# Kernel optimization log

Hardware: AMD Instinct MI355X
Metric: run time of the kernel (lower is better)

Reference implementation:

```python
import jax, jax.numpy as jnp
import numpy as np

N_NODES = 100000
N_EDGES = 800000
IN_F = 128
HID = 128
OUT_F = 64


def setup_inputs() -> dict:
    key = jax.random.key(0)
    ks = jax.random.split(key, 13)
    s = 1.0 / np.sqrt(HID)
    return {
        "x": jax.random.normal(ks[0], (N_NODES, IN_F), jnp.float32),
        "src": jax.random.randint(ks[1], (N_EDGES,), 0, N_NODES, jnp.int32),
        "dst": jax.random.randint(ks[2], (N_EDGES,), 0, N_NODES, jnp.int32),
        "W1": jax.random.normal(ks[3], (HID, IN_F), jnp.float32) * s,
        "b1": jax.random.normal(ks[4], (HID,), jnp.float32) * s,
        "W2": jax.random.normal(ks[5], (HID, HID), jnp.float32) * s,
        "b2": jax.random.normal(ks[6], (HID,), jnp.float32) * s,
        "W3": jax.random.normal(ks[7], (HID, HID), jnp.float32) * s,
        "b3": jax.random.normal(ks[8], (HID,), jnp.float32) * s,
        "Wo1": jax.random.normal(ks[9], (HID, HID), jnp.float32) * s,
        "bo1": jax.random.normal(ks[10], (HID,), jnp.float32) * s,
        "Wo2": jax.random.normal(ks[11], (OUT_F, HID), jnp.float32) * s,
        "bo2": jax.random.normal(ks[12], (OUT_F,), jnp.float32) * s,
    }


def _mean_agg(h, src, dst, n_nodes):
    # mean over incoming edges (DGL copy_u -> mean reducer); isolated nodes get 0
    summed = jax.ops.segment_sum(h[src], dst, num_segments=n_nodes)
    deg = jax.ops.segment_sum(jnp.ones_like(src, h.dtype), dst, num_segments=n_nodes)
    return summed / jnp.maximum(deg, 1.0)[:, None]


def _lin(h, W, b):
    return h @ W.T + b


def reference(x, src, dst, W1, b1, W2, b2, W3, b3, Wo1, bo1, Wo2, bo2):
    n = x.shape[0]
    # x1 = fc1(x); x = relu(x1); x2 = fc2(x)
    x2 = _lin(jax.nn.relu(_lin(x, W1, b1)), W2, b2)
    # gin1: apply_func = Sequential(fc1, relu, fc2) on (x2 + mean_agg(x2)), eps=0
    h = x2 + _mean_agg(x2, src, dst, n)
    h = _lin(jax.nn.relu(_lin(h, W1, b1)), W2, b2)
    # x3 = fc3(h); h = relu(x3)
    h = jax.nn.relu(_lin(h, W3, b3))
    # gin2: apply_func = Sequential(fc3, relu) on (h + mean_agg(h))
    h = h + _mean_agg(h, src, dst, n)
    h = jax.nn.relu(_lin(h, W3, b3))
    # output head
    h = jax.nn.relu(_lin(h, Wo1, bo1))
    return _lin(h, Wo2, bo2)
```

## Files before the change

kernel.cpp:

```cpp
#include <hip/hip_runtime.h>

#define NNODES 100000
#define NEDGES 800000
#define NTILE128 782
#define NROWPAD (NTILE128*128)

typedef _Float16 f16x8 __attribute__((ext_vector_type(8)));
typedef float    f32x4 __attribute__((ext_vector_type(4)));
typedef unsigned int u32;
typedef unsigned short u16;

__global__ __launch_bounds__(256) void hist_kernel(const int* __restrict__ dst,
                                                   int* __restrict__ counts, int nE) {
    int i = blockIdx.x * 256 + threadIdx.x;
    if (i < nE) atomicAdd(counts + dst[i], 1);
}

__global__ __launch_bounds__(256) void scan1_kernel(const int* __restrict__ counts,
                                                    int* __restrict__ bsum, int n) {
    __shared__ int s[256];
    int i = blockIdx.x * 256 + threadIdx.x;
    s[threadIdx.x] = (i < n) ? counts[i] : 0;
    __syncthreads();
    for (int off = 128; off > 0; off >>= 1) {
        if (threadIdx.x < off) s[threadIdx.x] += s[threadIdx.x + off];
        __syncthreads();
    }
    if (threadIdx.x == 0) bsum[blockIdx.x] = s[0];
}

__global__ __launch_bounds__(512) void scan2_kernel(int* __restrict__ bsum, int nb) {
    __shared__ int s[512];
    int t = threadIdx.x;
    int orig = (t < nb) ? bsum[t] : 0;
    s[t] = orig;
    __syncthreads();
    for (int off = 1; off < 512; off <<= 1) {
        int v = (t >= off) ? s[t - off] : 0;
        __syncthreads();
        s[t] += v;
        __syncthreads();
    }
    if (t < nb) bsum[t] = s[t] - orig;
}

__global__ __launch_bounds__(256) void scan3_kernel(int* __restrict__ counts,
                                                    const int* __restrict__ boff,
                                                    int* __restrict__ rowptr, int n) {
    __shared__ int s[256];
    int i = blockIdx.x * 256 + threadIdx.x;
    int t = threadIdx.x;
    int orig = (i < n) ? counts[i] : 0;
    s[t] = orig;
    __syncthreads();
    for (int off = 1; off < 256; off <<= 1) {
        int v = (t >= off) ? s[t - off] : 0;
        __syncthreads();
        s[t] += v;
        __syncthreads();
    }
    if (i < n) {
        rowptr[i] = boff[blockIdx.x] + s[t] - orig;
        counts[i] = 0;
    }
    if (i == n - 1) rowptr[n] = boff[blockIdx.x] + s[t];
}

__global__ __launch_bounds__(256) void fill_kernel(const int* __restrict__ src,
                                                   const int* __restrict__ dst,
                                                   const int* __restrict__ rowptr,
                                                   int* __restrict__ cur,
                                                   int* __restrict__ eidx, int nE) {
    int i = blockIdx.x * 256 + threadIdx.x;
    if (i >= nE) return;
    int d = dst[i];
    int p = atomicAdd(cur + d, 1);
    eidx[rowptr[d] + p] = src[i];
}

__global__ __launch_bounds__(256) void wpack_kernel(const float* __restrict__ W1,
                                                    const float* __restrict__ W2,
                                                    const float* __restrict__ W3,
                                                    const float* __restrict__ Wo1,
                                                    const float* __restrict__ Wo2,
                                                    _Float16* __restrict__ wp) {
    int i = blockIdx.x * 256 + threadIdx.x;
    if (i >= 9216) return;
    const float* Wm;
    int li;
    size_t base;
    if (i < 8192) {
        int m = i >> 11;
        li = i & 2047;
        Wm = (m == 0) ? W1 : (m == 1) ? W2 : (m == 2) ? W3 : Wo1;
        base = (size_t)m * 16384;
    } else {
        li = i - 8192;
        Wm = Wo2;
        base = 65536;
    }
    int lane = li & 63;
    int n = ((li >> 8) * 16) + (lane & 15);
    int k0 = (((li >> 6) & 3) * 32) + ((lane >> 4) * 8);
    const float* s = Wm + (size_t)n * 128 + k0;
    float4 a = *(const float4*)s;
    float4 b = *(const float4*)(s + 4);
    f16x8 v;
    v[0] = (_Float16)a.x; v[1] = (_Float16)a.y; v[2] = (_Float16)a.z; v[3] = (_Float16)a.w;
    v[4] = (_Float16)b.x; v[5] = (_Float16)b.y; v[6] = (_Float16)b.z; v[7] = (_Float16)b.w;
    *(f16x8*)(wp + base + (size_t)li * 8) = v;
}

__global__ __launch_bounds__(256) void gather_kernel(const _Float16* __restrict__ H,
                                                     const int* __restrict__ rowptr,
                                                     const int* __restrict__ eidx,
                                                     _Float16* __restrict__ O, int n) {
    int node = blockIdx.x * 4 + (threadIdx.x >> 6);
    int lane = threadIdx.x & 63;
    if (node >= n) return;
    int g = lane >> 4, p = lane & 15;
    int e0 = rowptr[node], e1 = rowptr[node + 1];
    float acc[8] = {0.f, 0.f, 0.f, 0.f, 0.f, 0.f, 0.f, 0.f};
    for (int j = e0; j < e1; j += 8) {
        int na = e1 - j;
        int sid = (lane < 8 && lane < na) ? eidx[j + lane] : -1;
        int s0 = __shfl(sid, g);
        int s1 = __shfl(sid, g + 4);
        f16x8 v0, v1;
        bool h0 = (s0 >= 0), h1 = (s1 >= 0);
        if (h0) v0 = *(const f16x8*)(H + (size_t)s0 * 128 + p * 8);
        if (h1) v1 = *(const f16x8*)(H + (size_t)s1 * 128 + p * 8);
        if (h0) {
#pragma unroll
            for (int r = 0; r < 8; ++r) acc[r] += (float)v0[r];
        }
        if (h1) {
#pragma unroll
            for (int r = 0; r < 8; ++r) acc[r] += (float)v1[r];
        }
    }
#pragma unroll
    for (int r = 0; r < 8; ++r) {
        acc[r] += __shfl_xor(acc[r], 16);
        acc[r] += __shfl_xor(acc[r], 32);
    }
    if (g == 0) {
        float rinv = 1.0f / fmaxf((float)(e1 - e0), 1.0f);
        f16x8 b = *(const f16x8*)(H + (size_t)node * 128 + p * 8);
        f16x8 o;
#pragma unroll
        for (int r = 0; r < 8; ++r) o[r] = (_Float16)((float)b[r] + acc[r] * rinv);
        *(f16x8*)(O + (size_t)node * 128 + p * 8) = o;
    }
}

template <int S, bool INF32, bool OUTF32, int TL, bool R0, bool R1, bool R2>
__global__ __launch_bounds__(512, 2) void chain_kernel(
    const void* __restrict__ A_,
    const _Float16* __restrict__ wq0, const float* __restrict__ Bg0,
    const _Float16* __restrict__ wq1, const float* __restrict__ Bg1,
    const _Float16* __restrict__ wq2, const float* __restrict__ Bg2,
    _Float16* __restrict__ O, float* __restrict__ Of32) {
    __shared__ u32 ibuf[128][137];
    const int tid = threadIdx.x;
    const int lane = tid & 63, w = tid >> 6;
    const int lm = lane & 15, g = lane >> 4;
    const int tile = blockIdx.x;

    f16x8 ah[4];
    const int arow = tile * 128 + w * 16 + lm;
    if (INF32) {
        const float* base = (const float*)A_ + (size_t)min(arow, NNODES - 1) * 128;
#pragma unroll
        for (int ks = 0; ks < 4; ++ks) {
            float4 a = *(const float4*)(base + ks * 32 + g * 8);
            float4 b = *(const float4*)(base + ks * 32 + g * 8 + 4);
            ah[ks][0] = (_Float16)a.x; ah[ks][1] = (_Float16)a.y;
            ah[ks][2] = (_Float16)a.z; ah[ks][3] = (_Float16)a.w;
            ah[ks][4] = (_Float16)b.x; ah[ks][5] = (_Float16)b.y;
            ah[ks][6] = (_Float16)b.z; ah[ks][7] = (_Float16)b.w;
        }
    } else {
        const _Float16* bp = (const _Float16*)A_ + (size_t)arow * 128;
#pragma unroll
        for (int ks = 0; ks < 4; ++ks) ah[ks] = *(const f16x8*)(bp + ks * 32 + g * 8);
    }

#pragma unroll
    for (int s = 0; s < S; ++s) {
        const _Float16* wq = (s == 0) ? wq0 : (s == 1) ? wq1 : wq2;
        const float* Bg = (s == 0) ? Bg0 : (s == 1) ? Bg1 : Bg2;
        const bool RELU = (s == 0) ? R0 : (s == 1) ? R1 : R2;
        const int T = (s == S - 1) ? TL : 8;

        f32x4 acc[8];
#pragma unroll
        for (int t = 0; t < 8; ++t)
            if (t < T) {
                float bv = Bg[t * 16 + lm];
                acc[t] = (f32x4){bv, bv, bv, bv};
            }
#pragma unroll
        for (int t = 0; t < 8; ++t)
            if (t < T) {
#pragma unroll
                for (int ks = 0; ks < 4; ++ks) {
                    f16x8 wv = *(const f16x8*)(wq + ((size_t)(t * 4 + ks) * 64 + lane) * 8);
                    acc[t] = __builtin_amdgcn_mfma_f32_16x16x32_f16(ah[ks], wv, acc[t], 0, 0, 0);
                }
            }

        if (s < S - 1) {
            __syncthreads();
            const int lrow0 = w * 16 + g * 4;
#pragma unroll
            for (int t = 0; t < 8; ++t)
#pragma unroll
                for (int r = 0; r < 4; ++r) {
                    float v = acc[t][r];
                    if (RELU) v = fmaxf(v, 0.f);
                    _Float16 h = (_Float16)v;
                    ibuf[lrow0 + r][t * 16 + lm] = (u32)(*(u16*)&h);
                }
            __syncthreads();
            const u32* rp = &ibuf[w * 16 + lm][0];
#pragma unroll
            for (int ks = 0; ks < 4; ++ks) {
                u32 v[8];
                *(f32x4*)v = *(const f32x4*)(rp + ks * 32 + g * 8);
                *(f32x4*)(v + 4) = *(const f32x4*)(rp + ks * 32 + g * 8 + 4);
#pragma unroll
                for (int j = 0; j < 8; ++j) {
                    u16 hs = (u16)(v[j] & 0xffffu);
                    ah[ks][j] = *(_Float16*)&hs;
                }
            }
        } else if (OUTF32) {
            const int mrow0 = tile * 128 + w * 16 + g * 4;
#pragma unroll
            for (int t = 0; t < TL; ++t) {
                const int n = t * 16 + lm;
#pragma unroll
                for (int r = 0; r < 4; ++r) {
                    float v = acc[t][r];
                    if (RELU) v = fmaxf(v, 0.f);
                    int m = mrow0 + r;
                    if (m < NNODES) Of32[(size_t)m * 64 + n] = v;
                }
            }
        } else {
            __syncthreads();
            const int lrow0 = w * 16 + g * 4;
#pragma unroll
            for (int t = 0; t < 8; ++t)
#pragma unroll
                for (int r = 0; r < 4; ++r) {
                    float v = acc[t][r];
                    if (RELU) v = fmaxf(v, 0.f);
                    _Float16 h = (_Float16)v;
                    ibuf[lrow0 + r][t * 16 + lm] = (u32)(*(u16*)&h);
                }
            __syncthreads();
#pragma unroll
            for (int pass = 0; pass < 4; ++pass) {
                int unit = pass * 512 + tid;
                int lrow = unit >> 4, c8 = unit & 15;
                const u32* p = &ibuf[lrow][c8 * 8];
                u32 v[8];
                *(f32x4*)v = *(const f32x4*)p;
                *(f32x4*)(v + 4) = *(const f32x4*)(p + 4);
                f16x8 hh;
#pragma unroll
                for (int j = 0; j < 8; ++j) {
                    u16 hs = (u16)(v[j] & 0xffffu);
                    hh[j] = *(_Float16*)&hs;
                }
                *(f16x8*)(O + (size_t)(tile * 128 + lrow) * 128 + c8 * 8) = hh;
            }
        }
    }
}

extern "C" void kernel_launch(void* const* d_in, const int* in_sizes, int n_in,
                              void* d_out, int out_size, void* d_ws, size_t ws_size,
                              hipStream_t stream) {
    const float* x   = (const float*)d_in[0];
    const int*   src = (const int*)d_in[1];
    const int*   dst = (const int*)d_in[2];
    const float* W1  = (const float*)d_in[3];
    const float* b1  = (const float*)d_in[4];
    const float* W2  = (const float*)d_in[5];
    const float* b2  = (const float*)d_in[6];
    const float* W3  = (const float*)d_in[7];
    const float* b3  = (const float*)d_in[8];
    const float* Wo1 = (const float*)d_in[9];
    const float* bo1 = (const float*)d_in[10];
    const float* Wo2 = (const float*)d_in[11];
    const float* bo2 = (const float*)d_in[12];
    float* out = (float*)d_out;

    const size_t PLANE = (size_t)NROWPAD * 128 * sizeof(_Float16);
    char* ws = (char*)d_ws;
    _Float16* P0 = (_Float16*)ws;
    _Float16* P1 = (_Float16*)(ws + PLANE);
    char* p = ws + 2 * PLANE;
    int* counts = (int*)p;     p += 512 * 1024;
    int* rowptr = (int*)p;     p += 512 * 1024;
    int* bsum   = (int*)p;     p += 16 * 1024;
    _Float16* wp = (_Float16*)p;  p += 256 * 1024;
    int* eidx   = (int*)p;

    dim3 blk(256);
    const int NB = (NNODES + 255) / 256;
    const int ge = (NEDGES + 255) / 256;
    const int gg = (NNODES + 3) / 4;

    wpack_kernel<<<36, blk, 0, stream>>>(W1, W2, W3, Wo1, Wo2, wp);

    hipMemsetAsync(counts, 0, NNODES * sizeof(int), stream);
    hist_kernel<<<ge, blk, 0, stream>>>(dst, counts, NEDGES);
    scan1_kernel<<<NB, blk, 0, stream>>>(counts, bsum, NNODES);
    scan2_kernel<<<1, 512, 0, stream>>>(bsum, NB);
    scan3_kernel<<<NB, blk, 0, stream>>>(counts, bsum, rowptr, NNODES);
    fill_kernel<<<ge, blk, 0, stream>>>(src, dst, rowptr, counts, eidx, NEDGES);

    const _Float16 *q1 = wp, *q2 = wp + 16384, *q3 = wp + 32768,
                   *qo1 = wp + 49152, *qo2 = wp + 65536;

    chain_kernel<2, true, false, 8, true, false, false><<<NTILE128, 512, 0, stream>>>(
        x, q1, b1, q2, b2, nullptr, nullptr, P0, nullptr);

    gather_kernel<<<gg, blk, 0, stream>>>(P0, rowptr, eidx, P1, NNODES);

    chain_kernel<3, false, false, 8, true, false, true><<<NTILE128, 512, 0, stream>>>(
        P1, q1, b1, q2, b2, q3, b3, P0, nullptr);

    gather_kernel<<<gg, blk, 0, stream>>>(P0, rowptr, eidx, P1, NNODES);

    chain_kernel<3, false, true, 4, true, true, false><<<NTILE128, 512, 0, stream>>>(
        P1, q3, b3, qo1, bo1, qo2, bo2, nullptr, out);
}
```

Before: 386.0 us.

## Build CSR via two-level bucket sort by 128-node tiles

Replaces the per-node histogram, three-stage scan and per-node atomic fill with a coarse histogram over 782 buckets of 128 nodes each. A single-block scan follows, then a staged scatter of packed (src, local dst) words per bucket. A per-bucket kernel then builds row pointers and the edge index using shared-memory atomics. This reduces global atomics on 100k counters and cuts kernel launches, at the cost of an extra 3.2MB staging pass and heavy contention on 782 global counters.

```diff
diff --git a/kernel.cpp b/kernel.cpp
--- a/kernel.cpp
+++ b/kernel.cpp
@@ -4,78 +4,84 @@
 #define NEDGES 800000
 #define NTILE128 782
 #define NROWPAD (NTILE128*128)
+#define NBKT 782
 
 typedef _Float16 f16x8 __attribute__((ext_vector_type(8)));
 typedef float    f32x4 __attribute__((ext_vector_type(4)));
 typedef unsigned int u32;
 typedef unsigned short u16;
 
-__global__ __launch_bounds__(256) void hist_kernel(const int* __restrict__ dst,
-                                                   int* __restrict__ counts, int nE) {
+__global__ __launch_bounds__(256) void chist_kernel(const int* __restrict__ dst,
+                                                    int* __restrict__ cb, int nE) {
     int i = blockIdx.x * 256 + threadIdx.x;
-    if (i < nE) atomicAdd(counts + dst[i], 1);
-}
-
-__global__ __launch_bounds__(256) void scan1_kernel(const int* __restrict__ counts,
-                                                    int* __restrict__ bsum, int n) {
-    __shared__ int s[256];
-    int i = blockIdx.x * 256 + threadIdx.x;
-    s[threadIdx.x] = (i < n) ? counts[i] : 0;
-    __syncthreads();
-    for (int off = 128; off > 0; off >>= 1) {
-        if (threadIdx.x < off) s[threadIdx.x] += s[threadIdx.x + off];
-        __syncthreads();
-    }
-    if (threadIdx.x == 0) bsum[blockIdx.x] = s[0];
-}
-
-__global__ __launch_bounds__(512) void scan2_kernel(int* __restrict__ bsum, int nb) {
-    __shared__ int s[512];
+    if (i < nE) atomicAdd(cb + (dst[i] >> 7), 1);
+}
+
+__global__ __launch_bounds__(1024) void cscan_kernel(const int* __restrict__ cb,
+                                                     int* __restrict__ cboff,
+                                                     int* __restrict__ ccur) {
+    __shared__ int s[1024];
     int t = threadIdx.x;
-    int orig = (t < nb) ? bsum[t] : 0;
-    s[t] = orig;
-    __syncthreads();
-    for (int off = 1; off < 512; off <<= 1) {
+    s[t] = (t < NBKT) ? cb[t] : 0;
+    __syncthreads();
+    for (int off = 1; off < 1024; off <<= 1) {
         int v = (t >= off) ? s[t - off] : 0;
         __syncthreads();
         s[t] += v;
         __syncthreads();
     }
-    if (t < nb) bsum[t] = s[t] - orig;
-}
-
-__global__ __launch_bounds__(256) void scan3_kernel(int* __restrict__ counts,
-                                                    const int* __restrict__ boff,
-                                                    int* __restrict__ rowptr, int n) {
-    __shared__ int s[256];
-    int i = blockIdx.x * 256 + threadIdx.x;
-    int t = threadIdx.x;
-    int orig = (i < n) ? counts[i] : 0;
-    s[t] = orig;
-    __syncthreads();
-    for (int off = 1; off < 256; off <<= 1) {
-        int v = (t >= off) ? s[t - off] : 0;
-        __syncthreads();
-        s[t] += v;
-        __syncthreads();
-    }
-    if (i < n) {
-        rowptr[i] = boff[blockIdx.x] + s[t] - orig;
-        counts[i] = 0;
-    }
-    if (i == n - 1) rowptr[n] = boff[blockIdx.x] + s[t];
-}
-
-__global__ __launch_bounds__(256) void fill_kernel(const int* __restrict__ src,
-                                                   const int* __restrict__ dst,
-                                                   const int* __restrict__ rowptr,
-                                                   int* __restrict__ cur,
-                                                   int* __restrict__ eidx, int nE) {
+    if (t < NBKT) {
+        cboff[t + 1] = s[t];
+        ccur[t] = 0;
+    }
+    if (t == 0) cboff[0] = 0;
+}
+
+__global__ __launch_bounds__(256) void fill1_kernel(const int* __restrict__ src,
+                                                    const int* __restrict__ dst,
+                                                    const int* __restrict__ cboff,
+                                                    int* __restrict__ ccur,
+                                                    u32* __restrict__ staged, int nE) {
     int i = blockIdx.x * 256 + threadIdx.x;
     if (i >= nE) return;
     int d = dst[i];
-    int p = atomicAdd(cur + d, 1);
-    eidx[rowptr[d] + p] = src[i];
+    int b = d >> 7;
+    int p = atomicAdd(ccur + b, 1);
+    staged[cboff[b] + p] = ((u32)src[i] << 7) | (u32)(d & 127);
+}
+
+__global__ __launch_bounds__(256) void fill2_kernel(const u32* __restrict__ staged,
+                                                    const int* __restrict__ cboff,
+                                                    int* __restrict__ rowptr,
+                                                    int* __restrict__ eidx) {
+    __shared__ int lcnt[128], lex[128], lcur[128];
+    int b = blockIdx.x, t = threadIdx.x;
+    int n0 = cboff[b], n1 = cboff[b + 1], cnt = n1 - n0;
+    if (t < 128) { lcnt[t] = 0; lcur[t] = 0; }
+    __syncthreads();
+    for (int j = t; j < cnt; j += 256) atomicAdd(&lcnt[staged[n0 + j] & 127], 1);
+    __syncthreads();
+    if (t < 128) lex[t] = lcnt[t];
+    __syncthreads();
+    for (int off = 1; off < 128; off <<= 1) {
+        int v = (t < 128 && t >= off) ? lex[t - off] : 0;
+        __syncthreads();
+        if (t < 128) lex[t] += v;
+        __syncthreads();
+    }
+    if (t < 128) {
+        int node = b * 128 + t;
+        int ex = lex[t] - lcnt[t];
+        if (node <= NNODES) rowptr[node] = n0 + ex;
+        lex[t] = ex;
+    }
+    __syncthreads();
+    for (int j = t; j < cnt; j += 256) {
+        u32 v = staged[n0 + j];
+        int dl = (int)(v & 127);
+        int p = atomicAdd(&lcur[dl], 1);
+        eidx[n0 + lex[dl] + p] = (int)(v >> 7);
+    }
 }
 
 __global__ __launch_bounds__(256) void wpack_kernel(const float* __restrict__ W1,
@@ -304,25 +310,25 @@
     _Float16* P0 = (_Float16*)ws;
     _Float16* P1 = (_Float16*)(ws + PLANE);
     char* p = ws + 2 * PLANE;
-    int* counts = (int*)p;     p += 512 * 1024;
-    int* rowptr = (int*)p;     p += 512 * 1024;
-    int* bsum   = (int*)p;     p += 16 * 1024;
+    int* rowptr = (int*)p;        p += 512 * 1024;
+    int* cb     = (int*)p;        p += 4 * 1024;
+    int* cboff  = (int*)p;        p += 4 * 1024;
+    int* ccur   = (int*)p;        p += 4 * 1024;
     _Float16* wp = (_Float16*)p;  p += 256 * 1024;
+    u32* staged = (u32*)p;        p += (size_t)NEDGES * 4;
     int* eidx   = (int*)p;
 
     dim3 blk(256);
-    const int NB = (NNODES + 255) / 256;
     const int ge = (NEDGES + 255) / 256;
     const int gg = (NNODES + 3) / 4;
 
     wpack_kernel<<<36, blk, 0, stream>>>(W1, W2, W3, Wo1, Wo2, wp);
 
-    hipMemsetAsync(counts, 0, NNODES * sizeof(int), stream);
-    hist_kernel<<<ge, blk, 0, stream>>>(dst, counts, NEDGES);
-    scan1_kernel<<<NB, blk, 0, stream>>>(counts, bsum, NNODES);
-    scan2_kernel<<<1, 512, 0, stream>>>(bsum, NB);
-    scan3_kernel<<<NB, blk, 0, stream>>>(counts, bsum, rowptr, NNODES);
-    fill_kernel<<<ge, blk, 0, stream>>>(src, dst, rowptr, counts, eidx, NEDGES);
+    hipMemsetAsync(cb, 0, NBKT * sizeof(int), stream);
+    chist_kernel<<<ge, blk, 0, stream>>>(dst, cb, NEDGES);
+    cscan_kernel<<<1, 1024, 0, stream>>>(cb, cboff, ccur);
+    fill1_kernel<<<ge, blk, 0, stream>>>(src, dst, cboff, ccur, staged, NEDGES);
+    fill2_kernel<<<NBKT, blk, 0, stream>>>(staged, cboff, rowptr, eidx);
 
     const _Float16 *q1 = wp, *q2 = wp + 16384, *q3 = wp + 32768,
                    *qo1 = wp + 49152, *qo2 = wp + 65536;
```

Measured after the change: 689.6 us. +78.6%, slower.
